# Performance work log

Hardware: AMD Instinct MI355X
Metric: run time of the kernel (lower is better)

Reference implementation:

```python
import jax, jax.numpy as jnp
import numpy as np

NUM_FRAMES = 8
NUM_HEADS = 12
NEG = -1e9


def _masks(N):
    i = jnp.arange(N)[:, None]
    j = jnp.arange(N)[None, :]
    b = NUM_FRAMES + 1  # boundary = 9
    head = (i < b) & (j < b)
    body = ((i >= b) & (j >= b)) | ((i == 0) & (j >= b)) | ((i >= b) & (j == 0)) | ((i == 0) & (j == 0))
    interact = ((i >= b) & (j < b)) | ((i < b) & (j >= b)) | ((i == 0) & (j == 0))
    return head, body, interact


def setup_inputs() -> dict:
    key = jax.random.key(0)
    k1, k2, k3 = jax.random.split(key, 3)
    B, N, C = 8, 1024, 768
    x = jax.random.normal(k1, (B, N, C), dtype=jnp.float32)
    w_qkv = jax.random.normal(k2, (3 * C, C), dtype=jnp.float32) * 0.02
    w_proj = jax.random.normal(k3, (C, C), dtype=jnp.float32) * 0.02
    b_proj = jnp.zeros((C,), dtype=jnp.float32)
    return {"x": x, "w_qkv": w_qkv, "w_proj": w_proj, "b_proj": b_proj}


def reference(x, w_qkv, w_proj, b_proj):
    B, N, C = x.shape
    H = NUM_HEADS
    hd = C // H
    scale = hd ** (-0.5)

    qkv = (x @ w_qkv.T).reshape(B, N, 3, H, hd).transpose(2, 0, 3, 1, 4)  # [3,B,H,N,hd]
    q, k, v = qkv[0], qkv[1], qkv[2]

    attn = jnp.einsum("bhnd,bhmd->bhnm", q, k) * scale  # [B,H,N,N]

    head_m, body_m, inter_m = _masks(N)

    def branch(mask):
        scores = jnp.where(mask, attn, NEG)
        p = jax.nn.softmax(scores, axis=-1)
        o = jnp.einsum("bhnm,bhmd->bhnd", p, v)  # [B,H,N,hd]
        o = o.transpose(0, 2, 1, 3).reshape(B, N, C)
        return o @ w_proj.T + b_proj

    return branch(head_m), branch(body_m), branch(inter_m)
```

## Files before the change

kernel.cpp:

```cpp
#include <hip/hip_runtime.h>
#include <stdint.h>

typedef unsigned short u16;
typedef unsigned int u32;
using f32x4 = __attribute__((ext_vector_type(4))) float;
using bf16x8 = __attribute__((ext_vector_type(8))) short;
using u16x8 = __attribute__((ext_vector_type(8))) unsigned short;
using u16x4 = __attribute__((ext_vector_type(4))) unsigned short;

#define QSCALE 0.18033688f

__device__ __forceinline__ u16 f2bf(float f) {
  u32 u = __float_as_uint(f);
  u32 r = (u + 0x7FFFu + ((u >> 16) & 1u)) >> 16;
  return (u16)r;
}
__device__ __forceinline__ float bf2f(u16 h) { return __uint_as_float(((u32)h) << 16); }

__device__ __forceinline__ void gload16(const void* g, void* l) {
  __builtin_amdgcn_global_load_lds((const __attribute__((address_space(1))) void*)g,
                                   (__attribute__((address_space(3))) void*)l, 16, 0, 0);
}

__global__ __launch_bounds__(256) void cvt_kernel(const float* __restrict__ src,
                                                  u16* __restrict__ dst, int n4) {
  int i = blockIdx.x * 256 + threadIdx.x;
  if (i < n4) {
    const float4 f = ((const float4*)src)[i];
    u16x4 o;
    o[0] = f2bf(f.x); o[1] = f2bf(f.y); o[2] = f2bf(f.z); o[3] = f2bf(f.w);
    ((u16x4*)dst)[i] = o;
  }
}

template <int MODE, int Mdim, int Ndim, int Kdim>
__global__ __launch_bounds__(256) void gemm_bt(const u16* __restrict__ A, const u16* __restrict__ Bw,
                                               u16* __restrict__ qb, u16* __restrict__ kb,
                                               u16* __restrict__ vTb,
                                               float* __restrict__ out, const float* __restrict__ bias) {
  __shared__ __align__(16) u16 lA[128 * 32];
  __shared__ __align__(16) u16 lB[128 * 32];
  const int tid = threadIdx.x;
  const int wid = tid >> 6, lane = tid & 63;
  const int m0 = blockIdx.x * 128, n0 = blockIdx.y * 128;
  const int wm = (wid >> 1) * 64, wn = (wid & 1) * 64;
  const int g = lane >> 4, r16 = lane & 15;

  f32x4 acc[4][4] = {};

  const int srow = wid * 16 + (lane >> 2);
  const int scol = (lane & 3) * 8;
  const u16* gA = A + (size_t)(m0 + srow) * Kdim + scol;
  const u16* gB = Bw + (size_t)(n0 + srow) * Kdim + scol;
  u16* lAw = lA + wid * 512;
  u16* lBw = lB + wid * 512;

  for (int k0 = 0; k0 < Kdim; k0 += 32) {
    gload16(gA + k0, lAw);
    gload16(gA + (size_t)64 * Kdim + k0, lAw + 2048);
    gload16(gB + k0, lBw);
    gload16(gB + (size_t)64 * Kdim + k0, lBw + 2048);
    __syncthreads();
    bf16x8 af[4], bfr[4];
#pragma unroll
    for (int i = 0; i < 4; ++i) af[i] = *(const bf16x8*)(lA + (wm + i * 16 + r16) * 32 + g * 8);
#pragma unroll
    for (int j = 0; j < 4; ++j) bfr[j] = *(const bf16x8*)(lB + (wn + j * 16 + r16) * 32 + g * 8);
#pragma unroll
    for (int i = 0; i < 4; ++i)
#pragma unroll
      for (int j = 0; j < 4; ++j)
        acc[i][j] = __builtin_amdgcn_mfma_f32_16x16x32_bf16(af[i], bfr[j], acc[i][j], 0, 0, 0);
    __syncthreads();
  }

#pragma unroll
  for (int i = 0; i < 4; ++i) {
    const int gm = m0 + wm + i * 16 + g * 4;
#pragma unroll
    for (int j = 0; j < 4; ++j) {
      const int gn = n0 + wn + j * 16 + r16;
      if constexpr (MODE == 1) {
        const float bv = bias[gn];
#pragma unroll
        for (int r = 0; r < 4; ++r) out[(size_t)(gm + r) * Ndim + gn] = acc[i][j][r] + bv;
      } else {
        const int t = gn / 768;
        const int rem = gn - t * 768;
        const int h = rem >> 6, d = rem & 63;
        if (t == 2) {
          u16x4 pk;
#pragma unroll
          for (int r = 0; r < 4; ++r) pk[r] = f2bf(acc[i][j][r]);
          const int b = gm >> 10, n = gm & 1023;
          *(u16x4*)(vTb + ((size_t)((b * 12 + h) * 64 + d)) * 1024 + n) = pk;
        } else {
          u16* dst = (t == 0) ? qb : kb;
          const float sc = (t == 0) ? QSCALE : 1.0f;
#pragma unroll
          for (int r = 0; r < 4; ++r) {
            const int b = (gm + r) >> 10, n = (gm + r) & 1023;
            dst[((size_t)((b * 12 + h) * 1024 + n)) * 64 + d] = f2bf(acc[i][j][r] * sc);
          }
        }
      }
    }
  }
}

__global__ __launch_bounds__(256) void vmean_kernel(const u16* __restrict__ vTb,
                                                    float* __restrict__ vmean) {
  const int bh = blockIdx.x, t = threadIdx.x;
  const int d = t >> 2, part = t & 3;
  const u16* src = vTb + ((size_t)bh * 64 + d) * 1024 + part * 256;
  float s = 0.f;
  for (int j = 0; j < 256; j += 8) {
    u16x8 u = *(const u16x8*)(src + j);
#pragma unroll
    for (int e = 0; e < 8; ++e) s += bf2f(u[e]);
  }
  s += __shfl_xor(s, 1);
  s += __shfl_xor(s, 2);
  if (part == 0) vmean[bh * 64 + d] = s * (1.0f / 1024.0f);
}

__global__ __launch_bounds__(256) void body_attn(const u16* __restrict__ qg, const u16* __restrict__ kg,
                                                 const u16* __restrict__ vg, const float* __restrict__ vmean,
                                                 u16* __restrict__ og) {
  __shared__ __align__(16) u16 lK[64 * 64];
  __shared__ __align__(16) u16 lV[64 * 64];
  __shared__ __align__(16) u16 lP[4][16 * 72];
  __shared__ float lsRed[4][16];

  const int blk = blockIdx.x;
  const int gid = (blk & 7) * 192 + (blk >> 3);
  const int rt = gid & 15, bh = gid >> 4;
  const int tid = threadIdx.x, wid = tid >> 6, lane = tid & 63;
  const int g = lane >> 4, r16 = lane & 15;
  const int row0 = rt * 64 + wid * 16;

  const u16* qrow = qg + ((size_t)bh * 1024 + row0 + r16) * 64;
  const bf16x8 aq0 = *(const bf16x8*)(qrow + g * 8);
  const bf16x8 aq1 = *(const bf16x8*)(qrow + 32 + g * 8);

  const int lrow = lane >> 3, lch = lane & 7;
  const int swz = (lch ^ lrow) * 8;
  const int j0 = wid * 2;
  const u16* gK = kg + (size_t)bh * 65536 + (size_t)(j0 * 8 + lrow) * 64 + swz;
  const u16* gV = vg + (size_t)bh * 65536 + (size_t)(j0 * 8 + lrow) * 1024 + swz;
  u16* lKd0 = lK + j0 * 512;
  u16* lKd1 = lK + (j0 + 1) * 512;
  u16* lVd0 = lV + j0 * 512;
  u16* lVd1 = lV + (j0 + 1) * 512;

  f32x4 oa[4] = {};
  float lsum = 0.f;
  u16* lPw = lP[wid];

  for (int c0 = 0; c0 < 1024; c0 += 64) {
    gload16(gK + (size_t)c0 * 64, lKd0);
    gload16(gK + (size_t)c0 * 64 + 512, lKd1);
    gload16(gV + c0, lVd0);
    gload16(gV + c0 + 8192, lVd1);
    __syncthreads();

#pragma unroll
    for (int kt = 0; kt < 4; ++kt) {
      const int key = kt * 16 + r16;
      const bf16x8 bk0 = *(const bf16x8*)(lK + key * 64 + ((g ^ (key & 7)) * 8));
      const bf16x8 bk1 = *(const bf16x8*)(lK + key * 64 + (((4 + g) ^ (key & 7)) * 8));
      f32x4 S = {};
      S = __builtin_amdgcn_mfma_f32_16x16x32_bf16(bk0, aq0, S, 0, 0, 0);
      S = __builtin_amdgcn_mfma_f32_16x16x32_bf16(bk1, aq1, S, 0, 0, 0);
      float p[4];
#pragma unroll
      for (int r = 0; r < 4; ++r) p[r] = exp2f(S[r]);
      if (c0 == 0 && kt == 0) {
        const int q = row0 + r16;
        const bool dropk0 = (q >= 1 && q <= 8);
#pragma unroll
        for (int r = 0; r < 4; ++r) {
          const int k = 4 * g + r;
          const bool keep = (k >= 9) || (k == 0 && !dropk0);
          p[r] = keep ? p[r] : 0.f;
        }
      }
      lsum += p[0] + p[1] + p[2] + p[3];
      u16x4 pk;
#pragma unroll
      for (int r = 0; r < 4; ++r) pk[r] = f2bf(p[r]);
      *(u16x4*)((char*)lPw + r16 * 144 + kt * 32 + g * 8) = pk;
    }
#pragma unroll
    for (int m = 0; m < 2; ++m) {
      const bf16x8 ap = *(const bf16x8*)((char*)lPw + r16 * 144 + m * 64 + g * 16);
#pragma unroll
      for (int jt = 0; jt < 4; ++jt) {
        const int d = jt * 16 + r16;
        const bf16x8 bv = *(const bf16x8*)(lV + d * 64 + (((m * 4 + g) ^ (d & 7)) * 8));
        oa[jt] = __builtin_amdgcn_mfma_f32_16x16x32_bf16(ap, bv, oa[jt], 0, 0, 0);
      }
    }
    __syncthreads();
  }

  lsum += __shfl_xor(lsum, 16);
  lsum += __shfl_xor(lsum, 32);
  if (lane < 16) lsRed[wid][lane] = lsum;

  const int b = bh / 12, h = bh - b * 12;
#pragma unroll
  for (int r = 0; r < 4; ++r) {
    const int grow = row0 + 4 * g + r;
    const bool full = (grow >= 1 && grow <= 8);
    const float inv = 1.f / lsRed[wid][4 * g + r];
#pragma unroll
    for (int jt = 0; jt < 4; ++jt) {
      const int d = jt * 16 + r16;
      const float vi = oa[jt][r] * inv;
      const float vb = full ? vmean[bh * 64 + d] : vi;
      og[((size_t)(8192 + b * 1024 + grow)) * 768 + h * 64 + d] = f2bf(vb);
      if (grow <= 8)
        og[((size_t)(16384 + b * 1024 + grow)) * 768 + h * 64 + d] = f2bf(vi);
    }
  }
}

__global__ __launch_bounds__(256) void smalls_attn(const u16* __restrict__ qg, const u16* __restrict__ kg,
                                                   const u16* __restrict__ vg, const float* __restrict__ vmean,
                                                   u16* __restrict__ og) {
  __shared__ __align__(16) u16 lP2[4][16 * 40];
  __shared__ float lsRed[4][16];
  const int bh = blockIdx.y;
  const int b = bh / 12, h = bh - b * 12;
  const int tid = threadIdx.x, wid = tid >> 6, lane = tid & 63;
  const int g = lane >> 4, r16 = lane & 15;
  u16* lPw = lP2[wid];

  const int row0 = blockIdx.x * 64 + wid * 16;
  const u16* qrow = qg + ((size_t)bh * 1024 + row0 + r16) * 64;
  const bf16x8 aq0 = *(const bf16x8*)(qrow + g * 8);
  const bf16x8 aq1 = *(const bf16x8*)(qrow + 32 + g * 8);
  const u16* krow = kg + ((size_t)bh * 1024 + r16) * 64;
  const bf16x8 bk0 = *(const bf16x8*)(krow + g * 8);
  const bf16x8 bk1 = *(const bf16x8*)(krow + 32 + g * 8);
  f32x4 S = {};
  S = __builtin_amdgcn_mfma_f32_16x16x32_bf16(bk0, aq0, S, 0, 0, 0);
  S = __builtin_amdgcn_mfma_f32_16x16x32_bf16(bk1, aq1, S, 0, 0, 0);
  float p[4];
  float lsum = 0.f;
#pragma unroll
  for (int r = 0; r < 4; ++r) {
    const int k = 4 * g + r;
    p[r] = (k < 9) ? exp2f(S[r]) : 0.f;
    lsum += p[r];
  }
  {
    u16x4 pk;
#pragma unroll
    for (int r = 0; r < 4; ++r) pk[r] = f2bf(p[r]);
    *(u16x4*)((char*)lPw + r16 * 80 + g * 8) = pk;
    u16x4 z = {0, 0, 0, 0};
    *(u16x4*)((char*)lPw + r16 * 80 + 32 + g * 8) = z;
  }
  lsum += __shfl_xor(lsum, 16);
  lsum += __shfl_xor(lsum, 32);
  if (lane < 16) lsRed[wid][lane] = lsum;
  const bf16x8 ap = *(const bf16x8*)((char*)lPw + r16 * 80 + g * 16);
  f32x4 oa[4] = {};
#pragma unroll
  for (int jt = 0; jt < 4; ++jt) {
    const u16* vrow = vg + ((size_t)bh * 64 + jt * 16 + r16) * 1024;
    const bf16x8 bv = *(const bf16x8*)(vrow + g * 8);
    oa[jt] = __builtin_amdgcn_mfma_f32_16x16x32_bf16(ap, bv, oa[jt], 0, 0, 0);
  }
#pragma unroll
  for (int r = 0; r < 4; ++r) {
    const int grow = row0 + 4 * g + r;
    const float inv = 1.f / lsRed[wid][4 * g + r];
#pragma unroll
    for (int jt = 0; jt < 4; ++jt) {
      const int d = jt * 16 + r16;
      const float v = oa[jt][r] * inv;
      if (grow >= 9) {
        og[((size_t)(16384 + b * 1024 + grow)) * 768 + h * 64 + d] = f2bf(v);
        og[((size_t)(b * 1024 + grow)) * 768 + h * 64 + d] = f2bf(vmean[bh * 64 + d]);
      } else {
        og[((size_t)(b * 1024 + grow)) * 768 + h * 64 + d] = f2bf(v);
      }
    }
  }
}

extern "C" void kernel_launch(void* const* d_in, const int* in_sizes, int n_in,
                              void* d_out, int out_size, void* d_ws, size_t ws_size,
                              hipStream_t stream) {
  (void)in_sizes; (void)n_in; (void)out_size; (void)ws_size;
  const float* x      = (const float*)d_in[0];
  const float* w_qkv  = (const float*)d_in[1];
  const float* w_proj = (const float*)d_in[2];
  const float* b_proj = (const float*)d_in[3];

  char* ws = (char*)d_ws;
  u16* xb     = (u16*)(ws + 0);
  u16* wqkvb  = (u16*)(ws + 12582912);
  u16* wprojb = (u16*)(ws + 16121856);
  u16* qb     = (u16*)(ws + 17301504);
  u16* kb     = (u16*)(ws + 29884416);
  u16* vTb    = (u16*)(ws + 42467328);
  float* vmn  = (float*)(ws + 55050240);
  u16* ob     = (u16*)(ws + 55074816);

  cvt_kernel<<<6144, 256, 0, stream>>>(x, xb, 1572864);
  cvt_kernel<<<1728, 256, 0, stream>>>(w_qkv, wqkvb, 442368);
  cvt_kernel<<<576, 256, 0, stream>>>(w_proj, wprojb, 147456);

  gemm_bt<0, 8192, 2304, 768><<<dim3(64, 18), 256, 0, stream>>>(
      xb, wqkvb, qb, kb, vTb, nullptr, nullptr);

  vmean_kernel<<<96, 256, 0, stream>>>(vTb, vmn);

  body_attn<<<1536, 256, 0, stream>>>(qb, kb, vTb, vmn, ob);
  smalls_attn<<<dim3(16, 96), 256, 0, stream>>>(qb, kb, vTb, vmn, ob);

  gemm_bt<1, 24576, 768, 768><<<dim3(192, 6), 256, 0, stream>>>(
      ob, wprojb, nullptr, nullptr, nullptr, (float*)d_out, b_proj);
}
```

Measured before the change: 194.4 us.

## Double-buffer LDS tiles in GEMM and body attention; merge conversion launches

```diff
diff --git a/kernel.cpp b/kernel.cpp
--- a/kernel.cpp
+++ b/kernel.cpp
@@ -22,15 +22,26 @@
                                    (__attribute__((address_space(3))) void*)l, 16, 0, 0);
 }
 
-__global__ __launch_bounds__(256) void cvt_kernel(const float* __restrict__ src,
-                                                  u16* __restrict__ dst, int n4) {
+__global__ __launch_bounds__(256) void cvt3_kernel(const float* __restrict__ a, u16* __restrict__ da, int n4a,
+                                                   const float* __restrict__ b, u16* __restrict__ db, int n4b,
+                                                   const float* __restrict__ c, u16* __restrict__ dc, int n4c) {
   int i = blockIdx.x * 256 + threadIdx.x;
-  if (i < n4) {
-    const float4 f = ((const float4*)src)[i];
-    u16x4 o;
-    o[0] = f2bf(f.x); o[1] = f2bf(f.y); o[2] = f2bf(f.z); o[3] = f2bf(f.w);
-    ((u16x4*)dst)[i] = o;
-  }
+  const float* src;
+  u16* dst;
+  int n;
+  if (i < n4a) {
+    src = a; dst = da; n = i;
+  } else if (i < n4a + n4b) {
+    src = b; dst = db; n = i - n4a;
+  } else if (i < n4a + n4b + n4c) {
+    src = c; dst = dc; n = i - n4a - n4b;
+  } else {
+    return;
+  }
+  const float4 f = ((const float4*)src)[n];
+  u16x4 o;
+  o[0] = f2bf(f.x); o[1] = f2bf(f.y); o[2] = f2bf(f.z); o[3] = f2bf(f.w);
+  ((u16x4*)dst)[n] = o;
 }
 
 template <int MODE, int Mdim, int Ndim, int Kdim>
@@ -38,8 +49,8 @@
                                                u16* __restrict__ qb, u16* __restrict__ kb,
                                                u16* __restrict__ vTb,
                                                float* __restrict__ out, const float* __restrict__ bias) {
-  __shared__ __align__(16) u16 lA[128 * 32];
-  __shared__ __align__(16) u16 lB[128 * 32];
+  __shared__ __align__(16) u16 lA[2][128 * 32];
+  __shared__ __align__(16) u16 lB[2][128 * 32];
   const int tid = threadIdx.x;
   const int wid = tid >> 6, lane = tid & 63;
   const int m0 = blockIdx.x * 128, n0 = blockIdx.y * 128;
@@ -52,26 +63,38 @@
   const int scol = (lane & 3) * 8;
   const u16* gA = A + (size_t)(m0 + srow) * Kdim + scol;
   const u16* gB = Bw + (size_t)(n0 + srow) * Kdim + scol;
-  u16* lAw = lA + wid * 512;
-  u16* lBw = lB + wid * 512;
-
+
+  gload16(gA, lA[0] + wid * 512);
+  gload16(gA + (size_t)64 * Kdim, lA[0] + wid * 512 + 2048);
+  gload16(gB, lB[0] + wid * 512);
+  gload16(gB + (size_t)64 * Kdim, lB[0] + wid * 512 + 2048);
+  __syncthreads();
+
+  int cur = 0;
   for (int k0 = 0; k0 < Kdim; k0 += 32) {
-    gload16(gA + k0, lAw);
-    gload16(gA + (size_t)64 * Kdim + k0, lAw + 2048);
-    gload16(gB + k0, lBw);
-    gload16(gB + (size_t)64 * Kdim + k0, lBw + 2048);
-    __syncthreads();
+    if (k0 + 32 < Kdim) {
+      const int nk = k0 + 32;
+      u16* lAn = lA[cur ^ 1] + wid * 512;
+      u16* lBn = lB[cur ^ 1] + wid * 512;
+      gload16(gA + nk, lAn);
+      gload16(gA + (size_t)64 * Kdim + nk, lAn + 2048);
+      gload16(gB + nk, lBn);
+      gload16(gB + (size_t)64 * Kdim + nk, lBn + 2048);
+    }
+    const u16* lAc = lA[cur];
+    const u16* lBc = lB[cur];
     bf16x8 af[4], bfr[4];
 #pragma unroll
-    for (int i = 0; i < 4; ++i) af[i] = *(const bf16x8*)(lA + (wm + i * 16 + r16) * 32 + g * 8);
-#pragma unroll
-    for (int j = 0; j < 4; ++j) bfr[j] = *(const bf16x8*)(lB + (wn + j * 16 + r16) * 32 + g * 8);
+    for (int i = 0; i < 4; ++i) af[i] = *(const bf16x8*)(lAc + (wm + i * 16 + r16) * 32 + g * 8);
+#pragma unroll
+    for (int j = 0; j < 4; ++j) bfr[j] = *(const bf16x8*)(lBc + (wn + j * 16 + r16) * 32 + g * 8);
 #pragma unroll
     for (int i = 0; i < 4; ++i)
 #pragma unroll
       for (int j = 0; j < 4; ++j)
         acc[i][j] = __builtin_amdgcn_mfma_f32_16x16x32_bf16(af[i], bfr[j], acc[i][j], 0, 0, 0);
     __syncthreads();
+    cur ^= 1;
   }
 
 #pragma unroll
@@ -127,8 +150,8 @@
 __global__ __launch_bounds__(256) void body_attn(const u16* __restrict__ qg, const u16* __restrict__ kg,
                                                  const u16* __restrict__ vg, const float* __restrict__ vmean,
                                                  u16* __restrict__ og) {
-  __shared__ __align__(16) u16 lK[64 * 64];
-  __shared__ __align__(16) u16 lV[64 * 64];
+  __shared__ __align__(16) u16 lK[2][64 * 64];
+  __shared__ __align__(16) u16 lV[2][64 * 64];
   __shared__ __align__(16) u16 lP[4][16 * 72];
   __shared__ float lsRed[4][16];
 
@@ -148,27 +171,34 @@
   const int j0 = wid * 2;
   const u16* gK = kg + (size_t)bh * 65536 + (size_t)(j0 * 8 + lrow) * 64 + swz;
   const u16* gV = vg + (size_t)bh * 65536 + (size_t)(j0 * 8 + lrow) * 1024 + swz;
-  u16* lKd0 = lK + j0 * 512;
-  u16* lKd1 = lK + (j0 + 1) * 512;
-  u16* lVd0 = lV + j0 * 512;
-  u16* lVd1 = lV + (j0 + 1) * 512;
 
   f32x4 oa[4] = {};
   float lsum = 0.f;
   u16* lPw = lP[wid];
 
+  gload16(gK, lK[0] + j0 * 512);
+  gload16(gK + 512, lK[0] + (j0 + 1) * 512);
+  gload16(gV, lV[0] + j0 * 512);
+  gload16(gV + 8192, lV[0] + (j0 + 1) * 512);
+  __syncthreads();
+
+  int cur = 0;
   for (int c0 = 0; c0 < 1024; c0 += 64) {
-    gload16(gK + (size_t)c0 * 64, lKd0);
-    gload16(gK + (size_t)c0 * 64 + 512, lKd1);
-    gload16(gV + c0, lVd0);
-    gload16(gV + c0 + 8192, lVd1);
-    __syncthreads();
+    if (c0 + 64 < 1024) {
+      const int nc = c0 + 64;
+      gload16(gK + (size_t)nc * 64, lK[cur ^ 1] + j0 * 512);
+      gload16(gK + (size_t)nc * 64 + 512, lK[cur ^ 1] + (j0 + 1) * 512);
+      gload16(gV + nc, lV[cur ^ 1] + j0 * 512);
+      gload16(gV + nc + 8192, lV[cur ^ 1] + (j0 + 1) * 512);
+    }
+    const u16* lKc = lK[cur];
+    const u16* lVc = lV[cur];
 
 #pragma unroll
     for (int kt = 0; kt < 4; ++kt) {
       const int key = kt * 16 + r16;
-      const bf16x8 bk0 = *(const bf16x8*)(lK + key * 64 + ((g ^ (key & 7)) * 8));
-      const bf16x8 bk1 = *(const bf16x8*)(lK + key * 64 + (((4 + g) ^ (key & 7)) * 8));
+      const bf16x8 bk0 = *(const bf16x8*)(lKc + key * 64 + ((g ^ (key & 7)) * 8));
+      const bf16x8 bk1 = *(const bf16x8*)(lKc + key * 64 + (((4 + g) ^ (key & 7)) * 8));
       f32x4 S = {};
       S = __builtin_amdgcn_mfma_f32_16x16x32_bf16(bk0, aq0, S, 0, 0, 0);
       S = __builtin_amdgcn_mfma_f32_16x16x32_bf16(bk1, aq1, S, 0, 0, 0);
@@ -197,11 +227,12 @@
 #pragma unroll
       for (int jt = 0; jt < 4; ++jt) {
         const int d = jt * 16 + r16;
-        const bf16x8 bv = *(const bf16x8*)(lV + d * 64 + (((m * 4 + g) ^ (d & 7)) * 8));
+        const bf16x8 bv = *(const bf16x8*)(lVc + d * 64 + (((m * 4 + g) ^ (d & 7)) * 8));
         oa[jt] = __builtin_amdgcn_mfma_f32_16x16x32_bf16(ap, bv, oa[jt], 0, 0, 0);
       }
     }
     __syncthreads();
+    cur ^= 1;
   }
 
   lsum += __shfl_xor(lsum, 16);
@@ -311,9 +342,7 @@
   float* vmn  = (float*)(ws + 55050240);
   u16* ob     = (u16*)(ws + 55074816);
 
-  cvt_kernel<<<6144, 256, 0, stream>>>(x, xb, 1572864);
-  cvt_kernel<<<1728, 256, 0, stream>>>(w_qkv, wqkvb, 442368);
-  cvt_kernel<<<576, 256, 0, stream>>>(w_proj, wprojb, 147456);
+  cvt3_kernel<<<8449, 256, 0, stream>>>(x, xb, 1572864, w_qkv, wqkvb, 442368, w_proj, wprojb, 147456);
 
   gemm_bt<0, 8192, 2304, 768><<<dim3(64, 18), 256, 0, stream>>>(
       xb, wqkvb, qb, kb, vTb, nullptr, nullptr);
```

After: 187.0 us. -3.8%, faster.
